# Optimization experiments

Hardware: AMD Instinct MI355X
Metric: run time of the kernel (lower is better)

Reference implementation:

```python
import jax, jax.numpy as jnp
import numpy as np

B, C, H, W = 32, 512, 56, 56
GROUPS = 32
CG = C // GROUPS  # channels per group = 16
EPS = 1e-5


def setup_inputs() -> dict:
    key = jax.random.key(0)
    ks = jax.random.split(key, 5)
    return {
        "x": jax.random.normal(ks[0], (B, C, H, W), jnp.float32),
        "w1": jax.random.normal(ks[1], (CG, CG), jnp.float32) * 0.1,   # conv1x1 weight [out,in]
        "b1": jax.random.normal(ks[2], (CG,), jnp.float32) * 0.1,
        "w3": jax.random.normal(ks[3], (CG, CG, 3, 3), jnp.float32) * 0.05,  # conv3x3 OIHW
        "b3": jax.random.normal(ks[4], (CG,), jnp.float32) * 0.1,
        "gn_w": jnp.ones((CG,), jnp.float32),
        "gn_b": jnp.zeros((CG,), jnp.float32),
    }


def reference(x, w1, b1, w3, b3, gn_w, gn_b):
    b, c, h, w = x.shape
    bg = b * GROUPS
    gx = x.reshape(bg, CG, h, w)                                  # group_x
    # directional pooling
    x_h = gx.mean(axis=3, keepdims=True)                          # [bg,cg,h,1]
    x_w = gx.mean(axis=2, keepdims=True).transpose(0, 1, 3, 2)    # [bg,cg,w,1]
    y = jnp.concatenate([x_h, x_w], axis=2)                       # [bg,cg,h+w,1]
    # conv1x1 == channel mixing
    y = jnp.einsum('oc,bcld->bold', w1, y) + b1[None, :, None, None]
    xh = jax.nn.sigmoid(y[:, :, :h])                              # [bg,cg,h,1]
    xw = jax.nn.sigmoid(y[:, :, h:].transpose(0, 1, 3, 2))        # [bg,cg,1,w]
    # GroupNorm(num_groups=cg, num_channels=cg) == per-channel instance norm
    x1 = gx * xh * xw
    mu = x1.mean(axis=(2, 3), keepdims=True)
    var = x1.var(axis=(2, 3), keepdims=True)
    x1 = (x1 - mu) * jax.lax.rsqrt(var + EPS) * gn_w[None, :, None, None] + gn_b[None, :, None, None]
    # conv3x3 branch
    x2 = jax.lax.conv_general_dilated(
        gx, w3, (1, 1), 'SAME',
        dimension_numbers=('NCHW', 'OIHW', 'NCHW')) + b3[None, :, None, None]
    # cross attention weights
    a1 = jax.nn.softmax(x1.mean(axis=(2, 3)), axis=-1)            # [bg,cg]
    a2 = jax.nn.softmax(x2.mean(axis=(2, 3)), axis=-1)            # [bg,cg]
    x1f = x1.reshape(bg, CG, h * w)
    x2f = x2.reshape(bg, CG, h * w)
    out1 = jnp.einsum('bc,bcl->bl', a1, x2f)                      # [bg,hw]
    out2 = jnp.einsum('bc,bcl->bl', a2, x1f)                      # [bg,hw]
    weights = (out1 + out2).reshape(bg, 1, h, w)
    out = gx * jax.nn.sigmoid(weights)
    return out.reshape(b, c, h, w)
```

## Files before the change

### kernel.cpp

```cpp
#include <hip/hip_runtime.h>
#include <math.h>

#define GROUPS 32
#define CG 16
#define HH 56
#define WW 56
#define HW (HH*WW)
#define BG 1024
#define EPS 1e-5f

#define RB 4
#define NB 14
#define NR (RB+2)
#define LROW 60
#define CPAD 4
#define CSTR (NR*LROW+CPAD)
#define XWS 60
#define XHS 57

#define U_ROW 0
#define U_COL 896
#define U_ST  1792
#define U_X2P 1936
#define U_LS1 2192
#define U_LS2 2208

__global__ __launch_bounds__(256, 4) void kF(const float* __restrict__ x,
        const float* __restrict__ w1, const float* __restrict__ b1,
        const float* __restrict__ w3, const float* __restrict__ b3,
        const float* __restrict__ gn_w, const float* __restrict__ gn_b,
        float* __restrict__ out)
{
    const int g = blockIdx.x;
    const int tid = threadIdx.x;
    const float* gx = x + (size_t)g * CG * HW;
    float* og = out + (size_t)g * CG * HW;

    __shared__ float s_u[CG * CSTR];
    __shared__ float s_xh[CG * XHS];
    __shared__ float s_xw[CG * XWS];
    __shared__ float s_wa[CG * 9 + 1];
    __shared__ float s_asc[CG];
    __shared__ float s_bias;

    if (tid < CG * 9 + 1) {
        float m = gn_b[0];
        #pragma unroll
        for (int c = 1; c < CG; ++c) m = fmaxf(m, gn_b[c]);
        float a1[CG]; float den = 0.f;
        #pragma unroll
        for (int c = 0; c < CG; ++c) { a1[c] = __expf(gn_b[c] - m); den += a1[c]; }
        float inv = 1.f / den;
        if (tid < CG * 9) {
            int ci = tid / 9, k = tid - (tid / 9) * 9;
            float s = 0.f;
            #pragma unroll
            for (int o = 0; o < CG; ++o) s += a1[o] * w3[(size_t)(o * CG + ci) * 9 + k];
            s_wa[tid] = s * inv;
        } else {
            float s = 0.f;
            #pragma unroll
            for (int o = 0; o < CG; ++o) s += a1[o] * b3[o];
            s_wa[CG * 9] = s * inv;
        }
    }

    {
        const int grp = tid >> 4;
        const int q   = tid & 15;
        const float* pc = gx + grp * HW;
        float c0 = 0.f, c1 = 0.f, c2 = 0.f, c3 = 0.f;
        #pragma unroll 2
        for (int row = 0; row < HH; row += 2) {
            float4 va = make_float4(0.f, 0.f, 0.f, 0.f);
            float4 vb = va;
            if (q < 14) {
                va = *(const float4*)(pc + row * WW + q * 4);
                vb = *(const float4*)(pc + (row + 1) * WW + q * 4);
            }
            c0 += va.x + vb.x; c1 += va.y + vb.y;
            c2 += va.z + vb.z; c3 += va.w + vb.w;
            float ra = (va.x + va.y) + (va.z + va.w);
            float rb = (vb.x + vb.y) + (vb.z + vb.w);
            ra += __shfl_down(ra, 8);  rb += __shfl_down(rb, 8);
            ra += __shfl_down(ra, 4);  rb += __shfl_down(rb, 4);
            ra += __shfl_down(ra, 2);  rb += __shfl_down(rb, 2);
            ra += __shfl_down(ra, 1);  rb += __shfl_down(rb, 1);
            if (q == 0) {
                s_u[U_ROW + grp * HH + row]     = ra * (1.0f / WW);
                s_u[U_ROW + grp * HH + row + 1] = rb * (1.0f / WW);
            }
        }
        if (q < 14) {
            s_u[U_COL + grp * WW + q * 4 + 0] = c0 * (1.0f / HH);
            s_u[U_COL + grp * WW + q * 4 + 1] = c1 * (1.0f / HH);
            s_u[U_COL + grp * WW + q * 4 + 2] = c2 * (1.0f / HH);
            s_u[U_COL + grp * WW + q * 4 + 3] = c3 * (1.0f / HH);
        }
    }
    __syncthreads();

    for (int t = tid; t < 2 * CG * HH; t += 256) {
        int hpart = (t < CG * HH);
        int tt = hpart ? t : t - CG * HH;
        int o = tt / HH, i = tt - (tt / HH) * HH;
        float v = b1[o];
        #pragma unroll
        for (int c = 0; c < CG; ++c)
            v += w1[o * CG + c] * (hpart ? s_u[U_ROW + c * HH + i]
                                         : s_u[U_COL + c * WW + i]);
        float sg = 1.f / (1.f + __expf(-v));
        if (hpart) s_xh[o * XHS + i] = sg;
        else       s_xw[o * XWS + i] = sg;
    }

    if (tid < CG) {
        const int c = tid;
        float S = 0.f;
        #pragma unroll
        for (int r = 0; r < HH; ++r) S += s_u[U_ROW + c * HH + r];
        float* st = &s_u[U_ST + c * 9];
        st[0] = S * (float)WW;
        st[1] = (float)WW * s_u[U_ROW + c * HH + HH - 1];
        st[2] = (float)WW * s_u[U_ROW + c * HH];
        st[3] = (float)HH * s_u[U_COL + c * WW + WW - 1];
        st[4] = (float)HH * s_u[U_COL + c * WW];
        const float* p = gx + c * HW;
        st[5] = p[0];
        st[6] = p[WW - 1];
        st[7] = p[(HH - 1) * WW];
        st[8] = p[(HH - 1) * WW + WW - 1];
    }
    __syncthreads();

    {
        const int o = tid >> 4, c = tid & 15;
        const float* wp = w3 + (size_t)(o * CG + c) * 9;
        const float* st = &s_u[U_ST + c * 9];
        float S = st[0];
        float acc = 0.f;
        #pragma unroll
        for (int dy = 0; dy < 3; ++dy) {
            float Rv = (dy == 0) ? st[1] : (dy == 2 ? st[2] : 0.f);
            #pragma unroll
            for (int dx = 0; dx < 3; ++dx) {
                float Cv = (dx == 0) ? st[3] : (dx == 2 ? st[4] : 0.f);
                float T = S - Rv - Cv;
                if (dy != 1 && dx != 1)
                    T += (dy == 0) ? ((dx == 0) ? st[8] : st[7])
                                   : ((dx == 0) ? st[6] : st[5]);
                acc += wp[dy * 3 + dx] * T;
            }
        }
        s_u[U_X2P + c * CG + o] = acc;
    }

    {
        const int c = tid >> 4;
        const int q = tid & 15;
        float s1 = 0.f, s2 = 0.f;
        if (q < 14) {
            const float* pc = gx + c * HW;
            float xw0 = s_xw[c * XWS + q * 4 + 0], xw1 = s_xw[c * XWS + q * 4 + 1];
            float xw2 = s_xw[c * XWS + q * 4 + 2], xw3v = s_xw[c * XWS + q * 4 + 3];
            #pragma unroll 4
            for (int row = 0; row < HH; ++row) {
                float4 v = *(const float4*)(pc + row * WW + q * 4);
                float xh = s_xh[c * XHS + row];
                float t0 = v.x * xh * xw0;
                float t1 = v.y * xh * xw1;
                float t2 = v.z * xh * xw2;
                float t3 = v.w * xh * xw3v;
                s1 += (t0 + t1) + (t2 + t3);
                s2 += (t0 * t0 + t1 * t1) + (t2 * t2 + t3 * t3);
            }
        }
        s1 += __shfl_down(s1, 8);  s2 += __shfl_down(s2, 8);
        s1 += __shfl_down(s1, 4);  s2 += __shfl_down(s2, 4);
        s1 += __shfl_down(s1, 2);  s2 += __shfl_down(s2, 2);
        s1 += __shfl_down(s1, 1);  s2 += __shfl_down(s2, 1);
        if (q == 0) { s_u[U_LS1 + c] = s1; s_u[U_LS2 + c] = s2; }
    }
    __syncthreads();

    if (tid < CG) {
        const int o = tid;
        float x2 = (float)HW * b3[o];
        #pragma unroll
        for (int c = 0; c < CG; ++c) x2 += s_u[U_X2P + c * CG + o];

        float mu  = s_u[U_LS1 + o] * (1.0f / HW);
        float var = s_u[U_LS2 + o] * (1.0f / HW) - mu * mu;
        float sc  = gn_w[o] * rsqrtf(var + EPS);
        float sh  = gn_b[o] - mu * sc;

        float v2 = x2 * (1.0f / HW);
        float m = v2;
        #pragma unroll
        for (int off = 8; off; off >>= 1) m = fmaxf(m, __shfl_xor(m, off));
        float e = __expf(v2 - m);
        float den = e;
        #pragma unroll
        for (int off = 8; off; off >>= 1) den += __shfl_xor(den, off);
        float a2 = e / den;

        s_asc[o] = a2 * sc;
        float part = a2 * sh;
        #pragma unroll
        for (int off = 8; off; off >>= 1) part += __shfl_xor(part, off);
        if (o == 0) s_bias = part + s_wa[CG * 9];
    }
    __syncthreads();

    if (tid < 96) {
        int c = tid / NR, r = tid - (tid / NR) * NR;
        *(float4*)&s_u[c * CSTR + r * LROW] = make_float4(0.f, 0.f, 0.f, 0.f);
    } else if (tid < 112) {
        int c = tid - 96;
        *(float4*)&s_u[c * CSTR + NR * LROW] = make_float4(0.f, 0.f, 0.f, 0.f);
    }
    for (int t = tid; t < CG * HH; t += 256) {
        int c = t / HH, y = t - (t / HH) * HH;
        s_xh[c * XHS + y] *= s_asc[c];
    }

    int cc = 0, ypr = 0, x0 = 0;
    float wreg[9];
    float xwv[8];
    if (tid < 224) {
        cc  = tid & 15;
        int sp = tid >> 4;
        ypr = sp / 7;
        x0  = (sp - ypr * 7) * 8;
        #pragma unroll
        for (int i = 0; i < 9; ++i) wreg[i] = s_wa[cc * 9 + i];
        float4 X0 = *(const float4*)&s_xw[cc * XWS + x0];
        float4 X1 = *(const float4*)&s_xw[cc * XWS + x0 + 4];
        xwv[0] = X0.x; xwv[1] = X0.y; xwv[2] = X0.z; xwv[3] = X0.w;
        xwv[4] = X1.x; xwv[5] = X1.y; xwv[6] = X1.z; xwv[7] = X1.w;
    }

    for (int band = 0; band < NB; ++band) {
        const int y0 = band * RB;

        for (int t = tid; t < CG * NR * 14; t += 256) {
            int c = t / (NR * 14);
            int rem = t - c * (NR * 14);
            int r = rem / 14, q = rem - r * 14;
            int ry = y0 - 1 + r;
            float4 v = make_float4(0.f, 0.f, 0.f, 0.f);
            if (ry >= 0 && ry < HH)
                v = *(const float4*)(gx + c * HW + ry * WW + 4 * q);
            *(float4*)&s_u[c * CSTR + r * LROW + 4 + 4 * q] = v;
        }
        __syncthreads();

        if (tid < 224) {
            float gh0 = s_xh[cc * XHS + y0 + 2 * ypr];
            float gh1 = s_xh[cc * XHS + y0 + 2 * ypr + 1];
            float g0[8], g1[8];
            #pragma unroll
            for (int j = 0; j < 8; ++j) { g0[j] = gh0 * xwv[j]; g1[j] = gh1 * xwv[j]; }

            float acc0[8], acc1[8];
            #pragma unroll
            for (int j = 0; j < 8; ++j) { acc0[j] = 0.f; acc1[j] = 0.f; }

            const int base = cc * CSTR + 2 * ypr * LROW + x0;
            #pragma unroll
            for (int rr = 0; rr < 4; ++rr) {
                const float* rp = &s_u[base + rr * LROW];
                float4 R0 = *(const float4*)(rp);
                float4 R1 = *(const float4*)(rp + 4);
                float4 R2 = *(const float4*)(rp + 8);
                float4 R3 = *(const float4*)(rp + 12);
                float win[10] = {R0.w, R1.x, R1.y, R1.z, R1.w,
                                 R2.x, R2.y, R2.z, R2.w, R3.x};
                if (rr < 3) {
                    float a0 = wreg[3 * rr], a1 = wreg[3 * rr + 1], a2 = wreg[3 * rr + 2];
                    #pragma unroll
                    for (int j = 0; j < 8; ++j)
                        acc0[j] += a0 * win[j] + a1 * win[j + 1] + a2 * win[j + 2];
                }
                if (rr > 0) {
                    float b0 = wreg[3 * (rr - 1)], b1v = wreg[3 * (rr - 1) + 1],
                          b2 = wreg[3 * (rr - 1) + 2];
                    #pragma unroll
                    for (int j = 0; j < 8; ++j)
                        acc1[j] += b0 * win[j] + b1v * win[j + 1] + b2 * win[j + 2];
                }
                if (rr == 1) {
                    #pragma unroll
                    for (int j = 0; j < 8; ++j) acc0[j] += g0[j] * win[j + 1];
                }
                if (rr == 2) {
                    #pragma unroll
                    for (int j = 0; j < 8; ++j) acc1[j] += g1[j] * win[j + 1];
                }
            }

            #pragma unroll
            for (int m = 1; m <= 8; m <<= 1) {
                #pragma unroll
                for (int j = 0; j < 8; ++j) {
                    acc0[j] += __shfl_xor(acc0[j], m);
                    acc1[j] += __shfl_xor(acc1[j], m);
                }
            }

            float bias = s_bias;
            float sg0[8], sg1[8];
            #pragma unroll
            for (int j = 0; j < 8; ++j) {
                sg0[j] = 1.f / (1.f + __expf(-(acc0[j] + bias)));
                sg1[j] = 1.f / (1.f + __expf(-(acc1[j] + bias)));
            }

            const float* c0p = &s_u[base + 1 * LROW + 4];
            const float* c1p = &s_u[base + 2 * LROW + 4];
            float4 C00 = *(const float4*)(c0p);
            float4 C01 = *(const float4*)(c0p + 4);
            float4 C10 = *(const float4*)(c1p);
            float4 C11 = *(const float4*)(c1p + 4);

            float* o0 = og + cc * HW + (y0 + 2 * ypr) * WW + x0;
            float* o1 = o0 + WW;
            *(float4*)(o0)     = make_float4(C00.x * sg0[0], C00.y * sg0[1],
                                             C00.z * sg0[2], C00.w * sg0[3]);
            *(float4*)(o0 + 4) = make_float4(C01.x * sg0[4], C01.y * sg0[5],
                                             C01.z * sg0[6], C01.w * sg0[7]);
            *(float4*)(o1)     = make_float4(C10.x * sg1[0], C10.y * sg1[1],
                                             C10.z * sg1[2], C10.w * sg1[3]);
            *(float4*)(o1 + 4) = make_float4(C11.x * sg1[4], C11.y * sg1[5],
                                             C11.z * sg1[6], C11.w * sg1[7]);
        }
        __syncthreads();
    }
}

extern "C" void kernel_launch(void* const* d_in, const int* in_sizes, int n_in,
                              void* d_out, int out_size, void* d_ws, size_t ws_size,
                              hipStream_t stream)
{
    const float* x    = (const float*)d_in[0];
    const float* w1   = (const float*)d_in[1];
    const float* b1   = (const float*)d_in[2];
    const float* w3   = (const float*)d_in[3];
    const float* b3   = (const float*)d_in[4];
    const float* gn_w = (const float*)d_in[5];
    const float* gn_b = (const float*)d_in[6];
    float* out = (float*)d_out;
    (void)d_ws; (void)ws_size;

    kF<<<BG, 256, 0, stream>>>(x, w1, b1, w3, b3, gn_w, gn_b, out);
}
```

Baseline: 476.8 us.

## Prefetch next band's input into registers while computing current band

Global loads for the next row band are issued into registers before the current band's compute, then written to LDS after a barrier. The index arithmetic for the staging loads is also precomputed once per thread. This is meant to hide global memory latency behind the compute phase. It adds 24 live registers per thread, which may spill or pressure occupancy under launch_bounds(256,4).

```diff
diff --git a/kernel.cpp b/kernel.cpp
--- a/kernel.cpp
+++ b/kernel.cpp
@@ -24,6 +24,8 @@
 #define U_X2P 1936
 #define U_LS1 2192
 #define U_LS2 2208
+
+#define NSTAGE (CG*NR*14)
 
 __global__ __launch_bounds__(256, 4) void kF(const float* __restrict__ x,
         const float* __restrict__ w1, const float* __restrict__ b1,
@@ -224,6 +226,43 @@
         s_xh[c * XHS + y] *= s_asc[c];
     }
 
+    const bool has6 = (tid < NSTAGE - 5 * 256);
+    int g_off[6], l_off[6], r_rel[6];
+    #pragma unroll
+    for (int i = 0; i < 6; ++i) {
+        int t = tid + i * 256;
+        if (t < NSTAGE) {
+            int c = t / (NR * 14);
+            int rem = t - c * (NR * 14);
+            int r = rem / 14, q = rem - r * 14;
+            r_rel[i] = r - 1;
+            g_off[i] = c * HW + (r - 1) * WW + 4 * q;
+            l_off[i] = c * CSTR + r * LROW + 4 + 4 * q;
+        } else {
+            r_rel[i] = 0; g_off[i] = 0; l_off[i] = 0;
+        }
+    }
+    float4 pf[6];
+
+    #define PREFETCH(BAND) do {                                            \
+        const int yb_ = (BAND) * RB;                                       \
+        _Pragma("unroll")                                                  \
+        for (int i = 0; i < 6; ++i) {                                      \
+            if (i < 5 || has6) {                                           \
+                int ry_ = yb_ + r_rel[i];                                  \
+                pf[i] = (ry_ >= 0 && ry_ < HH)                             \
+                    ? *(const float4*)(gx + g_off[i] + yb_ * WW)           \
+                    : make_float4(0.f, 0.f, 0.f, 0.f);                     \
+            }                                                              \
+        }                                                                  \
+    } while (0)
+
+    #define WRITELDS() do {                                                \
+        _Pragma("unroll")                                                  \
+        for (int i = 0; i < 6; ++i)                                        \
+            if (i < 5 || has6) *(float4*)&s_u[l_off[i]] = pf[i];           \
+    } while (0)
+
     int cc = 0, ypr = 0, x0 = 0;
     float wreg[9];
     float xwv[8];
@@ -240,20 +279,14 @@
         xwv[4] = X1.x; xwv[5] = X1.y; xwv[6] = X1.z; xwv[7] = X1.w;
     }
 
+    PREFETCH(0);
+    WRITELDS();
+    __syncthreads();
+
     for (int band = 0; band < NB; ++band) {
         const int y0 = band * RB;
 
-        for (int t = tid; t < CG * NR * 14; t += 256) {
-            int c = t / (NR * 14);
-            int rem = t - c * (NR * 14);
-            int r = rem / 14, q = rem - r * 14;
-            int ry = y0 - 1 + r;
-            float4 v = make_float4(0.f, 0.f, 0.f, 0.f);
-            if (ry >= 0 && ry < HH)
-                v = *(const float4*)(gx + c * HW + ry * WW + 4 * q);
-            *(float4*)&s_u[c * CSTR + r * LROW + 4 + 4 * q] = v;
-        }
-        __syncthreads();
+        if (band + 1 < NB) PREFETCH(band + 1);
 
         if (tid < 224) {
             float gh0 = s_xh[cc * XHS + y0 + 2 * ypr];
@@ -334,7 +367,12 @@
             *(float4*)(o1 + 4) = make_float4(C11.x * sg1[4], C11.y * sg1[5],
                                              C11.z * sg1[6], C11.w * sg1[7]);
         }
-        __syncthreads();
+
+        if (band + 1 < NB) {
+            __syncthreads();
+            WRITELDS();
+            __syncthreads();
+        }
     }
 }
 
```

After: 594.8 us. 1.25x slower.

## Use rolling six-row LDS ring and register-prefetch next band's rows

Applied to the files above, without the earlier changes.

The per-band reload of all six halo rows is replaced by a circular six-slot LDS row buffer. Only the four new rows per band are fetched from global memory into registers before the compute phase and written to LDS after it. This removes redundant reloading of the two overlapping halo rows and lets global load latency overlap with the stencil and sigmoid work. In exchange it adds an extra barrier per band, modulo slot indexing, and more register pressure under the 4-waves launch bound.

```diff
diff --git a/kernel.cpp b/kernel.cpp
--- a/kernel.cpp
+++ b/kernel.cpp
@@ -11,7 +11,7 @@
 
 #define RB 4
 #define NB 14
-#define NR (RB+2)
+#define NR 6
 #define LROW 60
 #define CPAD 4
 #define CSTR (NR*LROW+CPAD)
@@ -224,6 +224,55 @@
         s_xh[c * XHS + y] *= s_asc[c];
     }
 
+    for (int t = tid; t < CG * NR * 14; t += 256) {
+        int c = t / (NR * 14);
+        int rem = t - c * (NR * 14);
+        int r = rem / 14, q = rem - r * 14;
+        int ry = r - 1;
+        float4 v = make_float4(0.f, 0.f, 0.f, 0.f);
+        if (ry >= 0)
+            v = *(const float4*)(gx + c * HW + ry * WW + 4 * q);
+        *(float4*)&s_u[c * CSTR + r * LROW + 4 + 4 * q] = v;
+    }
+
+    const bool has4 = (tid < 128);
+    int gbase[4], lbase[4], rnew[4];
+    #pragma unroll
+    for (int i = 0; i < 4; ++i) {
+        int t = tid + i * 256;
+        if (t < 896) {
+            int c = t / 56;
+            int rem = t - c * 56;
+            int rn = rem / 14, q = rem - rn * 14;
+            rnew[i]  = rn;
+            gbase[i] = c * HW + 4 * q;
+            lbase[i] = c * CSTR + 4 + 4 * q;
+        } else { rnew[i] = 0; gbase[i] = 0; lbase[i] = 0; }
+    }
+    float4 pf[4];
+
+    #define PREFETCH(NBAND) do {                                           \
+        _Pragma("unroll")                                                  \
+        for (int i = 0; i < 4; ++i) {                                      \
+            if (i < 3 || has4) {                                           \
+                int row_ = (NBAND) * RB + 1 + rnew[i];                     \
+                pf[i] = (row_ < HH)                                        \
+                    ? *(const float4*)(gx + gbase[i] + row_ * WW)          \
+                    : make_float4(0.f, 0.f, 0.f, 0.f);                     \
+            }                                                              \
+        }                                                                  \
+    } while (0)
+
+    #define WRITELDS(NBAND) do {                                           \
+        _Pragma("unroll")                                                  \
+        for (int i = 0; i < 4; ++i) {                                      \
+            if (i < 3 || has4) {                                           \
+                int slot_ = ((NBAND) * RB + 2 + rnew[i]) % 6;              \
+                *(float4*)&s_u[lbase[i] + slot_ * LROW] = pf[i];           \
+            }                                                              \
+        }                                                                  \
+    } while (0)
+
     int cc = 0, ypr = 0, x0 = 0;
     float wreg[9];
     float xwv[8];
@@ -239,37 +288,30 @@
         xwv[0] = X0.x; xwv[1] = X0.y; xwv[2] = X0.z; xwv[3] = X0.w;
         xwv[4] = X1.x; xwv[5] = X1.y; xwv[6] = X1.z; xwv[7] = X1.w;
     }
+    __syncthreads();
 
     for (int band = 0; band < NB; ++band) {
         const int y0 = band * RB;
 
-        for (int t = tid; t < CG * NR * 14; t += 256) {
-            int c = t / (NR * 14);
-            int rem = t - c * (NR * 14);
-            int r = rem / 14, q = rem - r * 14;
-            int ry = y0 - 1 + r;
-            float4 v = make_float4(0.f, 0.f, 0.f, 0.f);
-            if (ry >= 0 && ry < HH)
-                v = *(const float4*)(gx + c * HW + ry * WW + 4 * q);
-            *(float4*)&s_u[c * CSTR + r * LROW + 4 + 4 * q] = v;
-        }
-        __syncthreads();
+        if (band + 1 < NB) PREFETCH(band + 1);
 
         if (tid < 224) {
             float gh0 = s_xh[cc * XHS + y0 + 2 * ypr];
             float gh1 = s_xh[cc * XHS + y0 + 2 * ypr + 1];
-            float g0[8], g1[8];
-            #pragma unroll
-            for (int j = 0; j < 8; ++j) { g0[j] = gh0 * xwv[j]; g1[j] = gh1 * xwv[j]; }
 
             float acc0[8], acc1[8];
             #pragma unroll
             for (int j = 0; j < 8; ++j) { acc0[j] = 0.f; acc1[j] = 0.f; }
 
-            const int base = cc * CSTR + 2 * ypr * LROW + x0;
+            const int ccx = cc * CSTR + x0;
+            const int sb = (y0 + 2 * ypr) % 6;
+            const float* rp1 = 0; const float* rp2 = 0;
             #pragma unroll
             for (int rr = 0; rr < 4; ++rr) {
-                const float* rp = &s_u[base + rr * LROW];
+                int slot = sb + rr; if (slot >= 6) slot -= 6;
+                const float* rp = &s_u[ccx + slot * LROW];
+                if (rr == 1) rp1 = rp;
+                if (rr == 2) rp2 = rp;
                 float4 R0 = *(const float4*)(rp);
                 float4 R1 = *(const float4*)(rp + 4);
                 float4 R2 = *(const float4*)(rp + 8);
@@ -291,11 +333,13 @@
                 }
                 if (rr == 1) {
                     #pragma unroll
-                    for (int j = 0; j < 8; ++j) acc0[j] += g0[j] * win[j + 1];
+                    for (int j = 0; j < 8; ++j)
+                        acc0[j] += gh0 * xwv[j] * win[j + 1];
                 }
                 if (rr == 2) {
                     #pragma unroll
-                    for (int j = 0; j < 8; ++j) acc1[j] += g1[j] * win[j + 1];
+                    for (int j = 0; j < 8; ++j)
+                        acc1[j] += gh1 * xwv[j] * win[j + 1];
                 }
             }
 
@@ -316,12 +360,10 @@
                 sg1[j] = 1.f / (1.f + __expf(-(acc1[j] + bias)));
             }
 
-            const float* c0p = &s_u[base + 1 * LROW + 4];
-            const float* c1p = &s_u[base + 2 * LROW + 4];
-            float4 C00 = *(const float4*)(c0p);
-            float4 C01 = *(const float4*)(c0p + 4);
-            float4 C10 = *(const float4*)(c1p);
-            float4 C11 = *(const float4*)(c1p + 4);
+            float4 C00 = *(const float4*)(rp1 + 4);
+            float4 C01 = *(const float4*)(rp1 + 8);
+            float4 C10 = *(const float4*)(rp2 + 4);
+            float4 C11 = *(const float4*)(rp2 + 8);
 
             float* o0 = og + cc * HW + (y0 + 2 * ypr) * WW + x0;
             float* o1 = o0 + WW;
@@ -334,7 +376,12 @@
             *(float4*)(o1 + 4) = make_float4(C11.x * sg1[4], C11.y * sg1[5],
                                              C11.z * sg1[6], C11.w * sg1[7]);
         }
-        __syncthreads();
+
+        if (band + 1 < NB) {
+            __syncthreads();
+            WRITELDS(band + 1);
+            __syncthreads();
+        }
     }
 }
 
```

Result: no change. 478.7 us (+0.4%).

## Replace LDS band staging with per-thread rolling register row windows

Applied to the files above, without the earlier changes.

Drops the shared-memory band loop that staged 6-row tiles with block-wide barriers. Each thread now walks down its own half of the image, loading rows straight from global into register windows and rotating them, so the per-band syncs and LDS traffic go away. The costs are more global loads per thread, including scalar halo loads that overlap between threads, and a smaller shared footprint. It also depends on L1/L2 to absorb redundant reads across the 16-channel lanes.

```diff
diff --git a/kernel.cpp b/kernel.cpp
--- a/kernel.cpp
+++ b/kernel.cpp
@@ -9,12 +9,6 @@
 #define BG 1024
 #define EPS 1e-5f
 
-#define RB 4
-#define NB 14
-#define NR (RB+2)
-#define LROW 60
-#define CPAD 4
-#define CSTR (NR*LROW+CPAD)
 #define XWS 60
 #define XHS 57
 
@@ -24,6 +18,7 @@
 #define U_X2P 1936
 #define U_LS1 2192
 #define U_LS2 2208
+#define U_SZ  2224
 
 __global__ __launch_bounds__(256, 4) void kF(const float* __restrict__ x,
         const float* __restrict__ w1, const float* __restrict__ b1,
@@ -36,7 +31,7 @@
     const float* gx = x + (size_t)g * CG * HW;
     float* og = out + (size_t)g * CG * HW;
 
-    __shared__ float s_u[CG * CSTR];
+    __shared__ float s_u[U_SZ];
     __shared__ float s_xh[CG * XHS];
     __shared__ float s_xw[CG * XWS];
     __shared__ float s_wa[CG * 9 + 1];
@@ -212,91 +207,74 @@
     }
     __syncthreads();
 
-    if (tid < 96) {
-        int c = tid / NR, r = tid - (tid / NR) * NR;
-        *(float4*)&s_u[c * CSTR + r * LROW] = make_float4(0.f, 0.f, 0.f, 0.f);
-    } else if (tid < 112) {
-        int c = tid - 96;
-        *(float4*)&s_u[c * CSTR + NR * LROW] = make_float4(0.f, 0.f, 0.f, 0.f);
-    }
     for (int t = tid; t < CG * HH; t += 256) {
         int c = t / HH, y = t - (t / HH) * HH;
         s_xh[c * XHS + y] *= s_asc[c];
     }
-
-    int cc = 0, ypr = 0, x0 = 0;
-    float wreg[9];
-    float xwv[8];
+    __syncthreads();
+
     if (tid < 224) {
-        cc  = tid & 15;
-        int sp = tid >> 4;
-        ypr = sp / 7;
-        x0  = (sp - ypr * 7) * 8;
+        const int cc   = tid & 15;
+        const int sp   = tid >> 4;
+        const int half = sp / 7;
+        const int x0   = (sp - half * 7) * 8;
+        const int ybase = half * 28;
+
+        float wreg[9];
         #pragma unroll
         for (int i = 0; i < 9; ++i) wreg[i] = s_wa[cc * 9 + i];
-        float4 X0 = *(const float4*)&s_xw[cc * XWS + x0];
-        float4 X1 = *(const float4*)&s_xw[cc * XWS + x0 + 4];
-        xwv[0] = X0.x; xwv[1] = X0.y; xwv[2] = X0.z; xwv[3] = X0.w;
-        xwv[4] = X1.x; xwv[5] = X1.y; xwv[6] = X1.z; xwv[7] = X1.w;
-    }
-
-    for (int band = 0; band < NB; ++band) {
-        const int y0 = band * RB;
-
-        for (int t = tid; t < CG * NR * 14; t += 256) {
-            int c = t / (NR * 14);
-            int rem = t - c * (NR * 14);
-            int r = rem / 14, q = rem - r * 14;
-            int ry = y0 - 1 + r;
-            float4 v = make_float4(0.f, 0.f, 0.f, 0.f);
-            if (ry >= 0 && ry < HH)
-                v = *(const float4*)(gx + c * HW + ry * WW + 4 * q);
-            *(float4*)&s_u[c * CSTR + r * LROW + 4 + 4 * q] = v;
-        }
-        __syncthreads();
-
-        if (tid < 224) {
-            float gh0 = s_xh[cc * XHS + y0 + 2 * ypr];
-            float gh1 = s_xh[cc * XHS + y0 + 2 * ypr + 1];
-            float g0[8], g1[8];
-            #pragma unroll
-            for (int j = 0; j < 8; ++j) { g0[j] = gh0 * xwv[j]; g1[j] = gh1 * xwv[j]; }
+        float xwv[8];
+        {
+            float4 X0 = *(const float4*)&s_xw[cc * XWS + x0];
+            float4 X1 = *(const float4*)&s_xw[cc * XWS + x0 + 4];
+            xwv[0] = X0.x; xwv[1] = X0.y; xwv[2] = X0.z; xwv[3] = X0.w;
+            xwv[4] = X1.x; xwv[5] = X1.y; xwv[6] = X1.z; xwv[7] = X1.w;
+        }
+        const float bias = s_bias;
+        const float* pc = gx + cc * HW + x0;
+        float* oc = og + cc * HW + x0;
+        const bool lok = (x0 > 0);
+        const bool rok = (x0 < 48);
+
+        float rw1[10], rw2[10], rw3[10], rw4[10];
+
+        #define LOADROW(R, W) do {                                         \
+            int r_ = (R);                                                  \
+            if (r_ >= 0 && r_ < HH) {                                      \
+                const float* bp_ = pc + r_ * WW;                           \
+                float4 f1_ = *(const float4*)(bp_);                        \
+                float4 f2_ = *(const float4*)(bp_ + 4);                    \
+                (W)[0] = lok ? bp_[-1] : 0.f;                              \
+                (W)[9] = rok ? bp_[8]  : 0.f;                              \
+                (W)[1] = f1_.x; (W)[2] = f1_.y; (W)[3] = f1_.z; (W)[4] = f1_.w; \
+                (W)[5] = f2_.x; (W)[6] = f2_.y; (W)[7] = f2_.z; (W)[8] = f2_.w; \
+            } else {                                                       \
+                _Pragma("unroll")                                          \
+                for (int i_ = 0; i_ < 10; ++i_) (W)[i_] = 0.f;             \
+            }                                                              \
+        } while (0)
+
+        LOADROW(ybase - 1, rw1);
+        LOADROW(ybase,     rw2);
+
+        for (int p = 0; p < 14; ++p) {
+            const int y0 = ybase + 2 * p;
+            LOADROW(y0 + 1, rw3);
+            LOADROW(y0 + 2, rw4);
+            const float gh0 = s_xh[cc * XHS + y0];
+            const float gh1 = s_xh[cc * XHS + y0 + 1];
 
             float acc0[8], acc1[8];
             #pragma unroll
-            for (int j = 0; j < 8; ++j) { acc0[j] = 0.f; acc1[j] = 0.f; }
-
-            const int base = cc * CSTR + 2 * ypr * LROW + x0;
-            #pragma unroll
-            for (int rr = 0; rr < 4; ++rr) {
-                const float* rp = &s_u[base + rr * LROW];
-                float4 R0 = *(const float4*)(rp);
-                float4 R1 = *(const float4*)(rp + 4);
-                float4 R2 = *(const float4*)(rp + 8);
-                float4 R3 = *(const float4*)(rp + 12);
-                float win[10] = {R0.w, R1.x, R1.y, R1.z, R1.w,
-                                 R2.x, R2.y, R2.z, R2.w, R3.x};
-                if (rr < 3) {
-                    float a0 = wreg[3 * rr], a1 = wreg[3 * rr + 1], a2 = wreg[3 * rr + 2];
-                    #pragma unroll
-                    for (int j = 0; j < 8; ++j)
-                        acc0[j] += a0 * win[j] + a1 * win[j + 1] + a2 * win[j + 2];
-                }
-                if (rr > 0) {
-                    float b0 = wreg[3 * (rr - 1)], b1v = wreg[3 * (rr - 1) + 1],
-                          b2 = wreg[3 * (rr - 1) + 2];
-                    #pragma unroll
-                    for (int j = 0; j < 8; ++j)
-                        acc1[j] += b0 * win[j] + b1v * win[j + 1] + b2 * win[j + 2];
-                }
-                if (rr == 1) {
-                    #pragma unroll
-                    for (int j = 0; j < 8; ++j) acc0[j] += g0[j] * win[j + 1];
-                }
-                if (rr == 2) {
-                    #pragma unroll
-                    for (int j = 0; j < 8; ++j) acc1[j] += g1[j] * win[j + 1];
-                }
+            for (int j = 0; j < 8; ++j) {
+                acc0[j] = wreg[0] * rw1[j] + wreg[1] * rw1[j + 1] + wreg[2] * rw1[j + 2]
+                        + wreg[3] * rw2[j] + wreg[4] * rw2[j + 1] + wreg[5] * rw2[j + 2]
+                        + wreg[6] * rw3[j] + wreg[7] * rw3[j + 1] + wreg[8] * rw3[j + 2]
+                        + gh0 * xwv[j] * rw2[j + 1];
+                acc1[j] = wreg[0] * rw2[j] + wreg[1] * rw2[j + 1] + wreg[2] * rw2[j + 2]
+                        + wreg[3] * rw3[j] + wreg[4] * rw3[j + 1] + wreg[5] * rw3[j + 2]
+                        + wreg[6] * rw4[j] + wreg[7] * rw4[j + 1] + wreg[8] * rw4[j + 2]
+                        + gh1 * xwv[j] * rw3[j + 1];
             }
 
             #pragma unroll
@@ -308,33 +286,23 @@
                 }
             }
 
-            float bias = s_bias;
-            float sg0[8], sg1[8];
+            float o0v[8], o1v[8];
             #pragma unroll
             for (int j = 0; j < 8; ++j) {
-                sg0[j] = 1.f / (1.f + __expf(-(acc0[j] + bias)));
-                sg1[j] = 1.f / (1.f + __expf(-(acc1[j] + bias)));
-            }
-
-            const float* c0p = &s_u[base + 1 * LROW + 4];
-            const float* c1p = &s_u[base + 2 * LROW + 4];
-            float4 C00 = *(const float4*)(c0p);
-            float4 C01 = *(const float4*)(c0p + 4);
-            float4 C10 = *(const float4*)(c1p);
-            float4 C11 = *(const float4*)(c1p + 4);
-
-            float* o0 = og + cc * HW + (y0 + 2 * ypr) * WW + x0;
+                o0v[j] = rw2[j + 1] * (1.f / (1.f + __expf(-(acc0[j] + bias))));
+                o1v[j] = rw3[j + 1] * (1.f / (1.f + __expf(-(acc1[j] + bias))));
+            }
+            float* o0 = oc + y0 * WW;
             float* o1 = o0 + WW;
-            *(float4*)(o0)     = make_float4(C00.x * sg0[0], C00.y * sg0[1],
-                                             C00.z * sg0[2], C00.w * sg0[3]);
-            *(float4*)(o0 + 4) = make_float4(C01.x * sg0[4], C01.y * sg0[5],
-                                             C01.z * sg0[6], C01.w * sg0[7]);
-            *(float4*)(o1)     = make_float4(C10.x * sg1[0], C10.y * sg1[1],
-                                             C10.z * sg1[2], C10.w * sg1[3]);
-            *(float4*)(o1 + 4) = make_float4(C11.x * sg1[4], C11.y * sg1[5],
-                                             C11.z * sg1[6], C11.w * sg1[7]);
-        }
-        __syncthreads();
+            *(float4*)(o0)     = make_float4(o0v[0], o0v[1], o0v[2], o0v[3]);
+            *(float4*)(o0 + 4) = make_float4(o0v[4], o0v[5], o0v[6], o0v[7]);
+            *(float4*)(o1)     = make_float4(o1v[0], o1v[1], o1v[2], o1v[3]);
+            *(float4*)(o1 + 4) = make_float4(o1v[4], o1v[5], o1v[6], o1v[7]);
+
+            #pragma unroll
+            for (int i = 0; i < 10; ++i) { rw1[i] = rw3[i]; rw2[i] = rw4[i]; }
+        }
+        #undef LOADROW
     }
 }
 
```

Result: slower. 491.7 us (+3.1%).
